# Kernel tuning notes

Measured on AMD Instinct MI355X. Metric: run time of the kernel, lower is better.

## Reference

```python
import jax, jax.numpy as jnp
import numpy as np

# Model constants (from init_kwargs)
C, T, H = 64, 64, 12          # num_channels, temporal_len, num_heads
BLOCK_IDX = 0                 # even -> temporal attention within each channel
QMAX = 127.0                  # symmetric int8


def fq(x):
    """Per-tensor symmetric int8 fake quantize-dequantize (Int8ActPerTensorFloat /
    Int8WeightPerTensorFloat style) with straight-through estimator."""
    s = jnp.maximum(jnp.max(jnp.abs(x)), 1e-8) / QMAX
    q = jnp.clip(jnp.round(x / s), -128.0, QMAX) * s
    return x + jax.lax.stop_gradient(q - x)


def layernorm(x, g, b):
    m = jnp.mean(x, axis=-1, keepdims=True)
    v = jnp.var(x, axis=-1, keepdims=True)
    return (x - m) * jax.lax.rsqrt(v + 1e-5) * g + b


def setup_inputs() -> dict:
    key = jax.random.key(0)
    ks = jax.random.split(key, 6)
    D = 768
    B = 8
    w = lambda k, shape: jax.random.normal(k, shape, jnp.float32) * 0.02
    return {
        "x": jax.random.normal(ks[0], (B, C * T, D), jnp.float32),
        "ln1_g": jnp.ones((D,), jnp.float32), "ln1_b": jnp.zeros((D,), jnp.float32),
        "qkv_w": w(ks[1], (3 * D, D)), "qkv_b": jnp.zeros((3 * D,), jnp.float32),
        "proj_w": w(ks[2], (D, D)), "proj_b": jnp.zeros((D,), jnp.float32),
        "ln2_g": jnp.ones((D,), jnp.float32), "ln2_b": jnp.zeros((D,), jnp.float32),
        "fc1_w": w(ks[3], (4 * D, D)), "fc1_b": jnp.zeros((4 * D,), jnp.float32),
        "fc2_w": w(ks[4], (D, 4 * D)), "fc2_b": jnp.zeros((D,), jnp.float32),
    }


def _attn(h, qkv_w, qkv_b, proj_w, proj_b):
    B, N, D = h.shape
    dh = D // H
    scale = 1.0 / np.sqrt(dh).astype(np.float32)
    # quantized qkv projection (input already fake-quanted, weights per-tensor int8)
    qkv = h @ fq(qkv_w).T + qkv_b                      # [B, N, 3D]
    qkv = qkv.reshape(B, C, T, 3, H, dh)
    if BLOCK_IDX % 2 == 0:
        # temporal attention: attend over T within each channel
        q, k, v = [qkv[:, :, :, i].transpose(0, 1, 3, 2, 4) for i in range(3)]  # [B,C,H,T,dh]
        scores = jnp.einsum("bchtd,bchsd->bchts", q, k) * scale
        p = jax.nn.softmax(scores, axis=-1)
        o = jnp.einsum("bchts,bchsd->bchtd", p, v)     # [B,C,H,T,dh]
        o = o.transpose(0, 1, 3, 2, 4).reshape(B, N, D)
    else:
        # channel attention: attend over C within each time step
        q, k, v = [qkv[:, :, :, i].transpose(0, 2, 3, 1, 4) for i in range(3)]  # [B,T,H,C,dh]
        scores = jnp.einsum("bthcd,bthed->bthce", q, k) * scale
        p = jax.nn.softmax(scores, axis=-1)
        o = jnp.einsum("bthce,bthed->bthcd", p, v)
        o = o.transpose(0, 3, 1, 2, 4).reshape(B, N, D)
    # quantized output projection
    return fq(o) @ fq(proj_w).T + proj_b


def reference(x, ln1_g, ln1_b, qkv_w, qkv_b, proj_w, proj_b,
              ln2_g, ln2_b, fc1_w, fc1_b, fc2_w, fc2_b):
    # attn branch
    h = fq(layernorm(x, ln1_g, ln1_b))                 # post_norm1_quant
    x = _attn(h, qkv_w, qkv_b, proj_w, proj_b) + x     # add1 residual
    # mlp branch
    h = fq(layernorm(x, ln2_g, ln2_b))                 # post_norm2_quant
    h = jax.nn.gelu(h @ fq(fc1_w).T + fc1_b, approximate=False)
    h = fq(h)                                          # post_gelu_quant
    return h @ fq(fc2_w).T + fc2_b + x                 # add2 residual
```

## Files before the change

kernel.cpp:

```cpp
#include <hip/hip_runtime.h>
#include <cmath>
#include <cstdint>

typedef _Float16 f16;
typedef _Float16 half8 __attribute__((ext_vector_type(8)));
typedef _Float16 half4 __attribute__((ext_vector_type(4)));
typedef float f32x4 __attribute__((ext_vector_type(4)));
typedef int i32x4 __attribute__((ext_vector_type(4)));
typedef int8_t c8v __attribute__((ext_vector_type(8)));
typedef int8_t c4v __attribute__((ext_vector_type(4)));

#define M_TOTAL 32768
#define D_MODEL 768
#define NE_TOT  25165824
#define SPREAD_STRIDE 16


__device__ __forceinline__ void async_copy16(void* lds, const void* gmem) {
  __builtin_amdgcn_global_load_lds(
      (__attribute__((address_space(1))) void*)gmem,
      (__attribute__((address_space(3))) void*)lds, 16, 0, 0);
}

__device__ __forceinline__ float gelu_fast(float v) {
  float x = v * 0.70710678118654752f;
  float ax = fabsf(x);
  float t = __builtin_amdgcn_rcpf(fmaf(0.3275911f, ax, 1.0f));
  float y = t * (0.254829592f +
            t * (-0.284496736f +
            t * (1.421413741f +
            t * (-1.453152027f + t * 1.061405429f))));
  float e = __expf(-x * x);
  float erf_ax = fmaf(-y, e, 1.0f);
  float erf_x = copysignf(erf_ax, x);
  return 0.5f * v * (1.0f + erf_x);
}

__device__ __forceinline__ float slot_scale(const unsigned* slot) {
  return fmaxf(__uint_as_float(*slot), 1e-8f) / 127.0f;
}

__device__ __forceinline__ int8_t q8_val(float v, float s) {
  float q = fminf(fmaxf(rintf(v / s), -128.f), 127.f);
  return (int8_t)(int)q;
}

template <int NW>
__device__ __forceinline__ float block_reduce_max_t(float m) {
  __shared__ float red_brm[NW];
  for (int o = 32; o; o >>= 1) m = fmaxf(m, __shfl_down(m, o));
  int lane = threadIdx.x & 63, wv = threadIdx.x >> 6;
  if (lane == 0) red_brm[wv] = m;
  __syncthreads();
  float r = red_brm[0];
#pragma unroll
  for (int w = 1; w < NW; ++w) r = fmaxf(r, red_brm[w]);
  return r;
}

__device__ __forceinline__ unsigned* spread_cell(unsigned* spread, int slot,
                                                 int cell) {
  return spread + slot * 64 * SPREAD_STRIDE + (cell & 63) * SPREAD_STRIDE;
}

__device__ __forceinline__ int xcd_swizzle(int lin, int nwg) {
  return (lin & 7) * (nwg >> 3) + (lin >> 3);
}

__device__ __forceinline__ void load_resid16(const float* resid, int N,
                                             int r0, int c0, float* rv) {
#pragma unroll
  for (int j = 0; j < 4; ++j)
#pragma unroll
    for (int reg = 0; reg < 4; ++reg)
      rv[j * 4 + reg] = resid[(size_t)(r0 + reg) * N + c0 + j * 16];
}


__global__ void zero_spread_k(unsigned* s) {
  int i = blockIdx.x * blockDim.x + threadIdx.x;
  if (i < 8 * 64 * SPREAD_STRIDE) s[i] = 0u;
}

__global__ void reduce_slots_k(const unsigned* __restrict__ spread,
                               unsigned* __restrict__ finals, int slot_lo,
                               int n_slots) {
  int wv = threadIdx.x >> 6, lane = threadIdx.x & 63;
  if (wv >= n_slots) return;
  int slot = slot_lo + wv;
  float m = __uint_as_float(spread[slot * 64 * SPREAD_STRIDE + lane * SPREAD_STRIDE]);
  for (int o = 32; o; o >>= 1) m = fmaxf(m, __shfl_down(m, o));
  if (lane == 0) finals[slot] = __float_as_uint(m);
}

__global__ __launch_bounds__(256) void absmax_k(const float* __restrict__ x,
                                                int n4, unsigned* spread,
                                                int slot) {
  int i = blockIdx.x * blockDim.x + threadIdx.x;
  int stride = gridDim.x * blockDim.x;
  float m = 0.f;
  const float4* x4 = (const float4*)x;
  for (; i < n4; i += stride) {
    float4 v = x4[i];
    m = fmaxf(m, fmaxf(fmaxf(fabsf(v.x), fabsf(v.y)),
                       fmaxf(fabsf(v.z), fabsf(v.w))));
  }
  m = block_reduce_max_t<4>(m);
  if (threadIdx.x == 0)
    atomicMax(spread_cell(spread, slot, blockIdx.x), __float_as_uint(m));
}

__global__ void quant_w8_k(const float* __restrict__ x, int n4,
                           const unsigned* __restrict__ slot,
                           int8_t* __restrict__ out) {
  int i = blockIdx.x * blockDim.x + threadIdx.x;
  if (i >= n4) return;
  float s = slot_scale(slot);
  float4 v = ((const float4*)x)[i];
  c4v q = {q8_val(v.x, s), q8_val(v.y, s), q8_val(v.z, s), q8_val(v.w, s)};
  ((c4v*)out)[i] = q;
}

__global__ __launch_bounds__(256) void ln_k(const float* __restrict__ x,
                                            const float* __restrict__ gw,
                                            const float* __restrict__ bw,
                                            f16* __restrict__ out,
                                            unsigned* spread, int slot) {
  int tid = threadIdx.x, lane = tid & 63, wv = tid >> 6;
  int row = blockIdx.x * 4 + wv;
  const float4* xr = (const float4*)(x + (size_t)row * D_MODEL);
  float4 v[3];
  float s = 0.f, ss = 0.f;
#pragma unroll
  for (int j = 0; j < 3; ++j) {
    v[j] = xr[lane + j * 64];
    s += v[j].x + v[j].y + v[j].z + v[j].w;
    ss += v[j].x * v[j].x + v[j].y * v[j].y + v[j].z * v[j].z +
          v[j].w * v[j].w;
  }
#pragma unroll
  for (int o = 32; o; o >>= 1) {
    s += __shfl_xor(s, o);
    ss += __shfl_xor(ss, o);
  }
  float mean = s * (1.f / 768.f);
  float var = ss * (1.f / 768.f) - mean * mean;
  float rstd = rsqrtf(var + 1e-5f);
  const float4* g4 = (const float4*)gw;
  const float4* b4 = (const float4*)bw;
  f16* outr = out + (size_t)row * D_MODEL;
  float m = 0.f;
#pragma unroll
  for (int j = 0; j < 3; ++j) {
    float4 g = g4[lane + j * 64], b = b4[lane + j * 64];
    float y0 = (v[j].x - mean) * rstd * g.x + b.x;
    float y1 = (v[j].y - mean) * rstd * g.y + b.y;
    float y2 = (v[j].z - mean) * rstd * g.z + b.z;
    float y3 = (v[j].w - mean) * rstd * g.w + b.w;
    half4 hq = {(f16)y0, (f16)y1, (f16)y2, (f16)y3};
    *(half4*)(outr + (size_t)(lane + j * 64) * 4) = hq;
    m = fmaxf(m, fmaxf(fmaxf(fabsf(y0), fabsf(y1)),
                       fmaxf(fabsf(y2), fabsf(y3))));
  }
#pragma unroll
  for (int o = 32; o; o >>= 1) m = fmaxf(m, __shfl_xor(m, o));
  if (lane == 0)
    atomicMax(spread_cell(spread, slot, blockIdx.x * 4 + wv),
              __float_as_uint(m));
}

__global__ void quant8_k(const f16* __restrict__ src, int n8,
                         const unsigned* __restrict__ slot,
                         int8_t* __restrict__ out) {
  int i = blockIdx.x * blockDim.x + threadIdx.x;
  if (i >= n8) return;
  float s = slot_scale(slot);
  half8 v = ((const half8*)src)[i];
  c8v q;
#pragma unroll
  for (int j = 0; j < 8; ++j) q[j] = q8_val((float)v[j], s);
  ((c8v*)out)[i] = q;
}

__global__ void quant_strided8_k(const f16* __restrict__ src,
                                 const unsigned* __restrict__ slot,
                                 int8_t* __restrict__ out) {
  int i = blockIdx.x * blockDim.x + threadIdx.x;
  if (i >= NE_TOT / 8) return;
  int row = i / 96, c8 = i - row * 96;
  half8 v = *(const half8*)(src + (size_t)row * 2304 + c8 * 8);
  float s = slot_scale(slot);
  c8v q;
#pragma unroll
  for (int j = 0; j < 8; ++j) q[j] = q8_val((float)v[j], s);
  ((c8v*)out)[i] = q;
}

template <int MODE>
__global__ __launch_bounds__(512) void gemm_i8_t(
    const int8_t* __restrict__ A, const int8_t* __restrict__ B,
    const unsigned* __restrict__ slotA, const unsigned* __restrict__ slotB,
    const float* __restrict__ bias, const float* resid,
    float* outf, f16* outh, unsigned* spread, int slot,
    int N, int K) {
  __shared__ __attribute__((aligned(16))) int8_t sA[3][128 * 128];
  __shared__ __attribute__((aligned(16))) int8_t sB[3][64 * 128];
  int tid = threadIdx.x;
  int nwg = gridDim.x * gridDim.y;
  int lin = blockIdx.y * gridDim.x + blockIdx.x;
  int swz = xcd_swizzle(lin, nwg);
  int n0 = (swz % gridDim.x) * 128, m0 = (swz / gridDim.x) * 256;
  int lane = tid & 63, wv = tid >> 6;
  int wm = (wv >> 1) * 64, wn = (wv & 1) * 64;
  int lr = lane & 15, quad = lane >> 4;

  i32x4 acc[4][4];
#pragma unroll
  for (int i = 0; i < 4; ++i)
#pragma unroll
    for (int j = 0; j < 4; ++j) acc[i][j] = i32x4{0, 0, 0, 0};

  auto mkA = [&](int c) {
    int pr = c >> 3, sl = c & 7, g = sl ^ (pr & 7);
    return A + (size_t)(m0 + 2 * pr + (g >> 2)) * K + (g & 3) * 16;
  };
  auto mkB = [&](int c) {
    int pr = c >> 3, sl = c & 7, g = sl ^ (pr & 7);
    return B + (size_t)(n0 + 2 * pr + (g >> 2)) * K + (g & 3) * 16;
  };
  const int8_t* sa0 = mkA(tid);
  const int8_t* sa1 = mkA(512 + tid);
  const int8_t* sb0 = mkB(tid);
  int la0 = tid * 16, la1 = (512 + tid) * 16;
  auto stage = [&](int b) {
    async_copy16(&sA[b][la0], sa0);
    async_copy16(&sA[b][la1], sa1);
    async_copy16(&sB[b][la0], sb0);
    sa0 += 64;
    sa1 += 64;
    sb0 += 64;
  };

  int aoff[4], boff[4];
#pragma unroll
  for (int i = 0; i < 4; ++i) {
    int r = wm + i * 16 + lr, pr = r >> 1;
    aoff[i] = pr * 128 + (((((r & 1) << 2) | quad) ^ (pr & 7)) * 16);
    int rb = wn + i * 16 + lr, prb = rb >> 1;
    boff[i] = prb * 128 + (((((rb & 1) << 2) | quad) ^ (prb & 7)) * 16);
  }
  auto compute = [&](const int8_t* a_s, const int8_t* b_s) {
    i32x4 af[4], bfv[4];
#pragma unroll
    for (int i = 0; i < 4; ++i) af[i] = *(const i32x4*)&a_s[aoff[i]];
#pragma unroll
    for (int j = 0; j < 4; ++j) bfv[j] = *(const i32x4*)&b_s[boff[j]];
#pragma unroll
    for (int i = 0; i < 4; ++i)
#pragma unroll
      for (int j = 0; j < 4; ++j)
        acc[i][j] = __builtin_amdgcn_mfma_i32_16x16x64_i8(af[i], bfv[j],
                                                          acc[i][j], 0, 0, 0);
  };

  int bi0 = 0, bi1 = 1, bi2 = 2;
  stage(bi0);
  stage(bi1);
  int nsteps = K >> 6;
  int pairs = nsteps >> 1;
  for (int S = 0; S < pairs; ++S) {
    bool last = (S == pairs - 1);
    if (!last) {
      stage(bi2);
      asm volatile("s_waitcnt vmcnt(6)" ::: "memory");
    } else {
      asm volatile("s_waitcnt vmcnt(3)" ::: "memory");
    }
    __builtin_amdgcn_s_barrier();
    compute(sA[bi0], sB[bi0]);
    __builtin_amdgcn_s_barrier();
    if (!last) {
      stage(bi0);
      asm volatile("s_waitcnt vmcnt(6)" ::: "memory");
    } else {
      asm volatile("s_waitcnt vmcnt(0)" ::: "memory");
    }
    __builtin_amdgcn_s_barrier();
    compute(sA[bi1], sB[bi1]);
    __builtin_amdgcn_s_barrier();
    int t = bi0;
    bi0 = bi2;
    bi2 = bi1;
    bi1 = t;
  }

  float scale = slot_scale(slotA) * slot_scale(slotB);
  int r0 = m0 + wm + quad * 4, c0 = n0 + wn + lr;
  float bv[4];
#pragma unroll
  for (int j = 0; j < 4; ++j) bv[j] = bias[c0 + j * 16];
  if (MODE == 2) {
    float rvA[16], rvB[16];
    load_resid16(resid, N, r0, c0, rvA);
#pragma unroll
    for (int i = 0; i < 4; ++i) {
      float* curv = (i & 1) ? rvB : rvA;
      float* nxt = (i & 1) ? rvA : rvB;
      if (i < 3) load_resid16(resid, N, r0 + (i + 1) * 16, c0, nxt);
#pragma unroll
      for (int j = 0; j < 4; ++j)
#pragma unroll
        for (int reg = 0; reg < 4; ++reg) {
          size_t idx = (size_t)(r0 + i * 16 + reg) * N + c0 + j * 16;
          outf[idx] = (float)acc[i][j][reg] * scale + bv[j] + curv[j * 4 + reg];
        }
    }
  } else if (MODE == 1) {
    float lmax = 0.f;
#pragma unroll
    for (int i = 0; i < 4; ++i)
#pragma unroll
      for (int j = 0; j < 4; ++j)
#pragma unroll
        for (int reg = 0; reg < 4; ++reg) {
          size_t idx = (size_t)(r0 + i * 16 + reg) * N + c0 + j * 16;
          float v = gelu_fast((float)acc[i][j][reg] * scale + bv[j]);
          lmax = fmaxf(lmax, fabsf(v));
          outh[idx] = (f16)v;
        }
    float bm = block_reduce_max_t<8>(lmax);
    if (tid == 0)
      atomicMax(spread_cell(spread, slot, blockIdx.x + gridDim.x * blockIdx.y),
                __float_as_uint(bm));
  } else {
#pragma unroll
    for (int i = 0; i < 4; ++i)
#pragma unroll
      for (int j = 0; j < 4; ++j)
#pragma unroll
        for (int reg = 0; reg < 4; ++reg) {
          size_t idx = (size_t)(r0 + i * 16 + reg) * N + c0 + j * 16;
          outh[idx] = (f16)((float)acc[i][j][reg] * scale + bv[j]);
        }
  }
}

__global__ __launch_bounds__(256) void attn_k(f16* __restrict__ qkv,
                                              unsigned* spread, int slot) {
  __shared__ __attribute__((aligned(16))) f16 sQ[64 * 72];
  __shared__ __attribute__((aligned(16))) f16 sK[64 * 72];
  __shared__ __attribute__((aligned(16))) f16 sV[64 * 72];
  __shared__ __attribute__((aligned(16))) f16 sP[64 * 72];
  int tid = threadIdx.x, lane = tid & 63, wv = tid >> 6;
  int lr = lane & 15, quad = lane >> 4;
  int swz = xcd_swizzle(blockIdx.x, gridDim.x);
  int h = swz % 12, bc = swz / 12;
  size_t base = (size_t)bc * 64 * 2304;
  int qo = h * 64, ko = qo + 768, vo = qo + 1536;

#pragma unroll
  for (int p = 0; p < 2; ++p) {
    int idx = p * 256 + tid;
    int t = idx >> 3, d8 = idx & 7;
    size_t g = base + (size_t)t * 2304 + d8 * 8;
    *(half8*)&sQ[t * 72 + d8 * 8] = *(const half8*)(qkv + g + qo);
    *(half8*)&sK[t * 72 + d8 * 8] = *(const half8*)(qkv + g + ko);
    *(half8*)&sV[t * 72 + d8 * 8] = *(const half8*)(qkv + g + vo);
  }
  __syncthreads();

  f32x4 acc[4];
#pragma unroll
  for (int j = 0; j < 4; ++j) acc[j] = f32x4{0.f, 0.f, 0.f, 0.f};
#pragma unroll
  for (int ks = 0; ks < 2; ++ks) {
    half8 aq = *(const half8*)&sQ[(wv * 16 + lr) * 72 + ks * 32 + quad * 8];
#pragma unroll
    for (int j = 0; j < 4; ++j) {
      half8 bk = *(const half8*)&sK[(j * 16 + lr) * 72 + ks * 32 + quad * 8];
      acc[j] = __builtin_amdgcn_mfma_f32_16x16x32_f16(aq, bk, acc[j], 0, 0, 0);
    }
  }

  float pr[4][4];
#pragma unroll
  for (int reg = 0; reg < 4; ++reg) {
    float v0 = acc[0][reg] * 0.125f, v1 = acc[1][reg] * 0.125f;
    float v2 = acc[2][reg] * 0.125f, v3 = acc[3][reg] * 0.125f;
    float mx = fmaxf(fmaxf(v0, v1), fmaxf(v2, v3));
    for (int o = 8; o; o >>= 1) mx = fmaxf(mx, __shfl_xor(mx, o));
    float e0 = __expf(v0 - mx), e1 = __expf(v1 - mx);
    float e2 = __expf(v2 - mx), e3 = __expf(v3 - mx);
    float sum = e0 + e1 + e2 + e3;
    for (int o = 8; o; o >>= 1) sum += __shfl_xor(sum, o);
    float inv = 1.f / sum;
    pr[0][reg] = e0 * inv; pr[1][reg] = e1 * inv;
    pr[2][reg] = e2 * inv; pr[3][reg] = e3 * inv;
  }
#pragma unroll
  for (int j = 0; j < 4; ++j)
#pragma unroll
    for (int reg = 0; reg < 4; ++reg)
      sP[(wv * 16 + quad * 4 + reg) * 72 + j * 16 + lr] = (f16)pr[j][reg];
  __syncthreads();

  f32x4 oacc[4];
#pragma unroll
  for (int j = 0; j < 4; ++j) oacc[j] = f32x4{0.f, 0.f, 0.f, 0.f};
#pragma unroll
  for (int ks = 0; ks < 2; ++ks) {
    half8 ap = *(const half8*)&sP[(wv * 16 + lr) * 72 + ks * 32 + quad * 8];
#pragma unroll
    for (int j = 0; j < 4; ++j) {
      half8 bv;
#pragma unroll
      for (int jj = 0; jj < 8; ++jj)
        bv[jj] = sV[(ks * 32 + quad * 8 + jj) * 72 + j * 16 + lr];
      oacc[j] = __builtin_amdgcn_mfma_f32_16x16x32_f16(ap, bv, oacc[j], 0, 0, 0);
    }
  }

  float lmax = 0.f;
#pragma unroll
  for (int j = 0; j < 4; ++j)
#pragma unroll
    for (int reg = 0; reg < 4; ++reg) {
      int m = wv * 16 + quad * 4 + reg;
      float v = oacc[j][reg];
      qkv[base + (size_t)m * 2304 + qo + j * 16 + lr] = (f16)v;
      lmax = fmaxf(lmax, fabsf(v));
    }
  lmax = block_reduce_max_t<4>(lmax);
  if (tid == 0)
    atomicMax(spread_cell(spread, slot, blockIdx.x), __float_as_uint(lmax));
}


extern "C" void kernel_launch(void* const* d_in, const int* in_sizes, int n_in,
                              void* d_out, int out_size, void* d_ws,
                              size_t ws_size, hipStream_t stream) {
  (void)in_sizes; (void)n_in; (void)out_size; (void)ws_size;
  const float* x      = (const float*)d_in[0];
  const float* ln1_g  = (const float*)d_in[1];
  const float* ln1_b  = (const float*)d_in[2];
  const float* qkv_w  = (const float*)d_in[3];
  const float* qkv_b  = (const float*)d_in[4];
  const float* proj_w = (const float*)d_in[5];
  const float* proj_b = (const float*)d_in[6];
  const float* ln2_g  = (const float*)d_in[7];
  const float* ln2_b  = (const float*)d_in[8];
  const float* fc1_w  = (const float*)d_in[9];
  const float* fc1_b  = (const float*)d_in[10];
  const float* fc2_w  = (const float*)d_in[11];
  const float* fc2_b  = (const float*)d_in[12];
  float* out = (float*)d_out;

  char* ws = (char*)d_ws;
  unsigned* spread = (unsigned*)ws;
  unsigned* finals = (unsigned*)(ws + 8 * 64 * SPREAD_STRIDE * 4);
  int8_t* qkv_wq  = (int8_t*)(ws + 33280);
  int8_t* proj_wq = qkv_wq + 1769472;
  int8_t* fc1_wq  = proj_wq + 589824;
  int8_t* fc2_wq  = fc1_wq + 2359296;
  int8_t* g_q  = fc2_wq + 2359296;
  f16*    hbuf = (f16*)g_q;
  int8_t* a_i8 = g_q + 50331648;
  f16*    big  = (f16*)(g_q + 100663296);

  zero_spread_k<<<(8 * 64 * SPREAD_STRIDE + 255) / 256, 256, 0, stream>>>(spread);

  absmax_k<<<256, 256, 0, stream>>>(qkv_w, 1769472 / 4, spread, 1);
  absmax_k<<<256, 256, 0, stream>>>(proj_w, 589824 / 4, spread, 2);
  absmax_k<<<256, 256, 0, stream>>>(fc1_w, 2359296 / 4, spread, 3);
  absmax_k<<<256, 256, 0, stream>>>(fc2_w, 2359296 / 4, spread, 4);
  reduce_slots_k<<<1, 256, 0, stream>>>(spread, finals, 1, 4);
  quant_w8_k<<<(1769472 / 4 + 255) / 256, 256, 0, stream>>>(qkv_w, 1769472 / 4, finals + 1, qkv_wq);
  quant_w8_k<<<(589824 / 4 + 255) / 256, 256, 0, stream>>>(proj_w, 589824 / 4, finals + 2, proj_wq);
  quant_w8_k<<<(2359296 / 4 + 255) / 256, 256, 0, stream>>>(fc1_w, 2359296 / 4, finals + 3, fc1_wq);
  quant_w8_k<<<(2359296 / 4 + 255) / 256, 256, 0, stream>>>(fc2_w, 2359296 / 4, finals + 4, fc2_wq);

  ln_k<<<8192, 256, 0, stream>>>(x, ln1_g, ln1_b, hbuf, spread, 0);
  reduce_slots_k<<<1, 64, 0, stream>>>(spread, finals, 0, 1);
  quant8_k<<<NE_TOT / 8 / 256, 256, 0, stream>>>(hbuf, NE_TOT / 8, finals + 0, a_i8);
  gemm_i8_t<0><<<dim3(18, 128), 512, 0, stream>>>(a_i8, qkv_wq, finals + 0, finals + 1,
                                                  qkv_b, nullptr, nullptr, big,
                                                  nullptr, 0, 2304, 768);
  attn_k<<<6144, 256, 0, stream>>>(big, spread, 5);
  reduce_slots_k<<<1, 64, 0, stream>>>(spread, finals, 5, 1);
  quant_strided8_k<<<NE_TOT / 8 / 256, 256, 0, stream>>>(big, finals + 5, a_i8);
  gemm_i8_t<2><<<dim3(6, 128), 512, 0, stream>>>(a_i8, proj_wq, finals + 5, finals + 2,
                                                 proj_b, x, out, nullptr,
                                                 nullptr, 0, 768, 768);
  ln_k<<<8192, 256, 0, stream>>>(out, ln2_g, ln2_b, hbuf, spread, 6);
  reduce_slots_k<<<1, 64, 0, stream>>>(spread, finals, 6, 1);
  quant8_k<<<NE_TOT / 8 / 256, 256, 0, stream>>>(hbuf, NE_TOT / 8, finals + 6, a_i8);
  gemm_i8_t<1><<<dim3(24, 128), 512, 0, stream>>>(a_i8, fc1_wq, finals + 6, finals + 3,
                                                  fc1_b, nullptr, nullptr, big,
                                                  spread, 7, 3072, 768);
  reduce_slots_k<<<1, 64, 0, stream>>>(spread, finals, 7, 1);
  quant8_k<<<100663296 / 8 / 256, 256, 0, stream>>>(big, 100663296 / 8, finals + 7, g_q);
  gemm_i8_t<2><<<dim3(6, 128), 512, 0, stream>>>(g_q, fc2_wq, finals + 7, finals + 4,
                                                 fc2_b, out, out, nullptr,
                                                 nullptr, 0, 768, 3072);
}
```

Baseline: 807.9 us.

## Fuse activation int8 quantization into GEMM A-operand loading

Removes the four standalone quantize kernels. The GEMM now loads fp16 activations straight from global memory into registers, quantizes them to int8 in-kernel with the per-tensor scale, and writes them to LDS, while B keeps its async LDS copies. This avoids writing and re-reading the int8 activation buffers. In exchange, the GEMM reads twice as many bytes for A, does extra conversion work inside the main loop, and drops from triple to double buffering for A, which can expose load latency.

```diff
diff --git a/kernel.cpp b/kernel.cpp
--- a/kernel.cpp
+++ b/kernel.cpp
@@ -7,7 +7,7 @@
 typedef _Float16 half4 __attribute__((ext_vector_type(4)));
 typedef float f32x4 __attribute__((ext_vector_type(4)));
 typedef int i32x4 __attribute__((ext_vector_type(4)));
-typedef int8_t c8v __attribute__((ext_vector_type(8)));
+typedef int8_t c16v __attribute__((ext_vector_type(16)));
 typedef int8_t c4v __attribute__((ext_vector_type(4)));
 
 #define M_TOTAL 32768
@@ -169,41 +169,15 @@
               __float_as_uint(m));
 }
 
-__global__ void quant8_k(const f16* __restrict__ src, int n8,
-                         const unsigned* __restrict__ slot,
-                         int8_t* __restrict__ out) {
-  int i = blockIdx.x * blockDim.x + threadIdx.x;
-  if (i >= n8) return;
-  float s = slot_scale(slot);
-  half8 v = ((const half8*)src)[i];
-  c8v q;
-#pragma unroll
-  for (int j = 0; j < 8; ++j) q[j] = q8_val((float)v[j], s);
-  ((c8v*)out)[i] = q;
-}
-
-__global__ void quant_strided8_k(const f16* __restrict__ src,
-                                 const unsigned* __restrict__ slot,
-                                 int8_t* __restrict__ out) {
-  int i = blockIdx.x * blockDim.x + threadIdx.x;
-  if (i >= NE_TOT / 8) return;
-  int row = i / 96, c8 = i - row * 96;
-  half8 v = *(const half8*)(src + (size_t)row * 2304 + c8 * 8);
-  float s = slot_scale(slot);
-  c8v q;
-#pragma unroll
-  for (int j = 0; j < 8; ++j) q[j] = q8_val((float)v[j], s);
-  ((c8v*)out)[i] = q;
-}
-
 template <int MODE>
-__global__ __launch_bounds__(512) void gemm_i8_t(
-    const int8_t* __restrict__ A, const int8_t* __restrict__ B,
+__global__ __launch_bounds__(512) void gemm_q_t(
+    const f16* __restrict__ A, int lda,
+    const int8_t* __restrict__ B,
     const unsigned* __restrict__ slotA, const unsigned* __restrict__ slotB,
     const float* __restrict__ bias, const float* resid,
     float* outf, f16* outh, unsigned* spread, int slot,
     int N, int K) {
-  __shared__ __attribute__((aligned(16))) int8_t sA[3][128 * 128];
+  __shared__ __attribute__((aligned(16))) int8_t sA[2][128 * 128];
   __shared__ __attribute__((aligned(16))) int8_t sB[3][64 * 128];
   int tid = threadIdx.x;
   int nwg = gridDim.x * gridDim.y;
@@ -214,6 +188,9 @@
   int wm = (wv >> 1) * 64, wn = (wv & 1) * 64;
   int lr = lane & 15, quad = lane >> 4;
 
+  float sa = slot_scale(slotA);
+  float inv = 1.0f / sa;
+
   i32x4 acc[4][4];
 #pragma unroll
   for (int i = 0; i < 4; ++i)
@@ -222,23 +199,46 @@
 
   auto mkA = [&](int c) {
     int pr = c >> 3, sl = c & 7, g = sl ^ (pr & 7);
-    return A + (size_t)(m0 + 2 * pr + (g >> 2)) * K + (g & 3) * 16;
-  };
+    return A + (size_t)(m0 + 2 * pr + (g >> 2)) * lda + (g & 3) * 16;
+  };
+  const f16* pa0 = mkA(tid);
+  const f16* pa1 = mkA(512 + tid);
+  int la0 = tid * 16, la1 = (512 + tid) * 16;
+
   auto mkB = [&](int c) {
     int pr = c >> 3, sl = c & 7, g = sl ^ (pr & 7);
     return B + (size_t)(n0 + 2 * pr + (g >> 2)) * K + (g & 3) * 16;
   };
-  const int8_t* sa0 = mkA(tid);
-  const int8_t* sa1 = mkA(512 + tid);
   const int8_t* sb0 = mkB(tid);
-  int la0 = tid * 16, la1 = (512 + tid) * 16;
-  auto stage = [&](int b) {
-    async_copy16(&sA[b][la0], sa0);
-    async_copy16(&sA[b][la1], sa1);
-    async_copy16(&sB[b][la0], sb0);
-    sa0 += 64;
-    sa1 += 64;
+  auto gloadB = [&](int8_t* buf) {
+    async_copy16(buf + la0, sb0);
     sb0 += 64;
+  };
+
+  float4 ra0, ra1, ra2, ra3;
+  float4 rb0, rb1, rb2, rb3;
+  auto issueA0 = [&]() {
+    ra0 = *(const float4*)pa0; ra1 = *(const float4*)(pa0 + 8);
+    ra2 = *(const float4*)pa1; ra3 = *(const float4*)(pa1 + 8);
+    pa0 += 64; pa1 += 64;
+  };
+  auto issueA1 = [&]() {
+    rb0 = *(const float4*)pa0; rb1 = *(const float4*)(pa0 + 8);
+    rb2 = *(const float4*)pa1; rb3 = *(const float4*)(pa1 + 8);
+    pa0 += 64; pa1 += 64;
+  };
+  auto q16 = [&](float4 lo, float4 hi) -> c16v {
+    half8 h0 = *(half8*)&lo;
+    half8 h1 = *(half8*)&hi;
+    c16v q;
+#pragma unroll
+    for (int e = 0; e < 8; ++e) {
+      float v0 = (float)h0[e] * inv;
+      float v1 = (float)h1[e] * inv;
+      q[e] = (int8_t)(int)fminf(fmaxf(rintf(v0), -128.f), 127.f);
+      q[8 + e] = (int8_t)(int)fminf(fmaxf(rintf(v1), -128.f), 127.f);
+    }
+    return q;
   };
 
   int aoff[4], boff[4];
@@ -263,38 +263,50 @@
                                                           acc[i][j], 0, 0, 0);
   };
 
-  int bi0 = 0, bi1 = 1, bi2 = 2;
-  stage(bi0);
-  stage(bi1);
+  int8_t* pb0 = sB[0];
+  int8_t* pb1 = sB[1];
+  int8_t* pb2 = sB[2];
+  gloadB(pb0);
+  issueA0();
+  gloadB(pb1);
+  issueA1();
   int nsteps = K >> 6;
   int pairs = nsteps >> 1;
   for (int S = 0; S < pairs; ++S) {
-    bool last = (S == pairs - 1);
-    if (!last) {
-      stage(bi2);
+    bool lastp = (S == pairs - 1);
+    if (!lastp) {
+      gloadB(pb2);
       asm volatile("s_waitcnt vmcnt(6)" ::: "memory");
     } else {
-      asm volatile("s_waitcnt vmcnt(3)" ::: "memory");
-    }
+      asm volatile("s_waitcnt vmcnt(5)" ::: "memory");
+    }
+    *(c16v*)&sA[0][la0] = q16(ra0, ra1);
+    *(c16v*)&sA[0][la1] = q16(ra2, ra3);
+    if (!lastp) issueA0();
+    asm volatile("s_waitcnt lgkmcnt(0)" ::: "memory");
     __builtin_amdgcn_s_barrier();
-    compute(sA[bi0], sB[bi0]);
+    compute(sA[0], pb0);
     __builtin_amdgcn_s_barrier();
-    if (!last) {
-      stage(bi0);
+    if (!lastp) {
+      gloadB(pb0);
       asm volatile("s_waitcnt vmcnt(6)" ::: "memory");
     } else {
       asm volatile("s_waitcnt vmcnt(0)" ::: "memory");
     }
+    *(c16v*)&sA[1][la0] = q16(rb0, rb1);
+    *(c16v*)&sA[1][la1] = q16(rb2, rb3);
+    if (!lastp) issueA1();
+    asm volatile("s_waitcnt lgkmcnt(0)" ::: "memory");
     __builtin_amdgcn_s_barrier();
-    compute(sA[bi1], sB[bi1]);
+    compute(sA[1], pb1);
     __builtin_amdgcn_s_barrier();
-    int t = bi0;
-    bi0 = bi2;
-    bi2 = bi1;
-    bi1 = t;
-  }
-
-  float scale = slot_scale(slotA) * slot_scale(slotB);
+    int8_t* t = pb0;
+    pb0 = pb2;
+    pb2 = pb1;
+    pb1 = t;
+  }
+
+  float scale = sa * slot_scale(slotB);
   int r0 = m0 + wm + quad * 4, c0 = n0 + wn + lr;
   float bv[4];
 #pragma unroll
@@ -462,10 +474,8 @@
   int8_t* proj_wq = qkv_wq + 1769472;
   int8_t* fc1_wq  = proj_wq + 589824;
   int8_t* fc2_wq  = fc1_wq + 2359296;
-  int8_t* g_q  = fc2_wq + 2359296;
-  f16*    hbuf = (f16*)g_q;
-  int8_t* a_i8 = g_q + 50331648;
-  f16*    big  = (f16*)(g_q + 100663296);
+  f16* hbuf = (f16*)(fc2_wq + 2359296);
+  f16* big  = (f16*)((char*)hbuf + 50331648);
 
   zero_spread_k<<<(8 * 64 * SPREAD_STRIDE + 255) / 256, 256, 0, stream>>>(spread);
 
@@ -481,25 +491,25 @@
 
   ln_k<<<8192, 256, 0, stream>>>(x, ln1_g, ln1_b, hbuf, spread, 0);
   reduce_slots_k<<<1, 64, 0, stream>>>(spread, finals, 0, 1);
-  quant8_k<<<NE_TOT / 8 / 256, 256, 0, stream>>>(hbuf, NE_TOT / 8, finals + 0, a_i8);
-  gemm_i8_t<0><<<dim3(18, 128), 512, 0, stream>>>(a_i8, qkv_wq, finals + 0, finals + 1,
-                                                  qkv_b, nullptr, nullptr, big,
-                                                  nullptr, 0, 2304, 768);
+  gemm_q_t<0><<<dim3(18, 128), 512, 0, stream>>>(hbuf, 768, qkv_wq,
+                                                 finals + 0, finals + 1,
+                                                 qkv_b, nullptr, nullptr, big,
+                                                 nullptr, 0, 2304, 768);
   attn_k<<<6144, 256, 0, stream>>>(big, spread, 5);
   reduce_slots_k<<<1, 64, 0, stream>>>(spread, finals, 5, 1);
-  quant_strided8_k<<<NE_TOT / 8 / 256, 256, 0, stream>>>(big, finals + 5, a_i8);
-  gemm_i8_t<2><<<dim3(6, 128), 512, 0, stream>>>(a_i8, proj_wq, finals + 5, finals + 2,
-                                                 proj_b, x, out, nullptr,
-                                                 nullptr, 0, 768, 768);
+  gemm_q_t<2><<<dim3(6, 128), 512, 0, stream>>>(big, 2304, proj_wq,
+                                                finals + 5, finals + 2,
+                                                proj_b, x, out, nullptr,
+                                                nullptr, 0, 768, 768);
   ln_k<<<8192, 256, 0, stream>>>(out, ln2_g, ln2_b, hbuf, spread, 6);
   reduce_slots_k<<<1, 64, 0, stream>>>(spread, finals, 6, 1);
-  quant8_k<<<NE_TOT / 8 / 256, 256, 0, stream>>>(hbuf, NE_TOT / 8, finals + 6, a_i8);
-  gemm_i8_t<1><<<dim3(24, 128), 512, 0, stream>>>(a_i8, fc1_wq, finals + 6, finals + 3,
-                                                  fc1_b, nullptr, nullptr, big,
-                                                  spread, 7, 3072, 768);
+  gemm_q_t<1><<<dim3(24, 128), 512, 0, stream>>>(hbuf, 768, fc1_wq,
+                                                 finals + 6, finals + 3,
+                                                 fc1_b, nullptr, nullptr, big,
+                                                 spread, 7, 3072, 768);
   reduce_slots_k<<<1, 64, 0, stream>>>(spread, finals, 7, 1);
-  quant8_k<<<100663296 / 8 / 256, 256, 0, stream>>>(big, 100663296 / 8, finals + 7, g_q);
-  gemm_i8_t<2><<<dim3(6, 128), 512, 0, stream>>>(g_q, fc2_wq, finals + 7, finals + 4,
-                                                 fc2_b, out, out, nullptr,
-                                                 nullptr, 0, 768, 3072);
-}
+  gemm_q_t<2><<<dim3(6, 128), 512, 0, stream>>>(big, 3072, fc2_wq,
+                                                finals + 7, finals + 4,
+                                                fc2_b, out, out, nullptr,
+                                                nullptr, 0, 768, 3072);
+}
```

Measured after the change: 1.029 ms. 1.27x slower.
